# Kernel tuning notes

Hardware: AMD Instinct MI355X
Metric: run time of the kernel (lower is better)

Reference implementation:

```python
import jax, jax.numpy as jnp
import numpy as np

E = 3_200_000
H = 8
N = 100_000

def setup_inputs() -> dict:
    key = jax.random.key(0)
    k1, k2 = jax.random.split(key)
    logits = jax.random.normal(k1, (E, H, 1), dtype=jnp.float32)
    dst = jax.random.randint(k2, (E,), 0, N, dtype=jnp.int32)
    return {"logits": logits, "dst": dst, "num_nodes": N}

def reference(logits, dst, num_nodes):
    # block_compute(copy_edge, max): segmented max of edge logits per dst node -> [M, H, 1]
    max_logits = jax.ops.segment_max(logits, dst, num_segments=num_nodes)
    # apply_block: exp(z_ij - max_i) per edge (gather dst max back to edges)
    scores = jnp.exp(logits - max_logits[dst])  # [E, H, 1]
    # block_compute(copy_edge, sum): segmented sum of exp'd scores per dst node -> [M, H, 1]
    normalizer = jax.ops.segment_sum(scores, dst, num_segments=num_nodes)
    return scores, normalizer
```

## Files before the change

kernel.cpp:

```cpp
#include <hip/hip_runtime.h>


__device__ __forceinline__ unsigned enc_f32(float f) {
    unsigned u = __float_as_uint(f);
    return (u & 0x80000000u) ? ~u : (u | 0x80000000u);
}
__device__ __forceinline__ float dec_f32(unsigned u) {
    return __uint_as_float((u & 0x80000000u) ? (u & 0x7FFFFFFFu) : ~u);
}

template <int H>
__global__ void smax_k(const float* __restrict__ logits,
                       const int* __restrict__ dst,
                       unsigned* __restrict__ menc, int EH) {
    int i = blockIdx.x * blockDim.x + threadIdx.x;
    if (i >= EH) return;
    int e = i / H;
    int h = i - e * H;
    int d = dst[e];
    atomicMax(menc + d * H + h, enc_f32(logits[i]));
}

__global__ void smax_g(const float* __restrict__ logits,
                       const int* __restrict__ dst,
                       unsigned* __restrict__ menc, int EH, int H) {
    int i = blockIdx.x * blockDim.x + threadIdx.x;
    if (i >= EH) return;
    int e = i / H;
    int h = i - e * H;
    int d = dst[e];
    atomicMax(menc + d * H + h, enc_f32(logits[i]));
}

template <int H>
__global__ void score_k(const float* __restrict__ logits,
                        const int* __restrict__ dst,
                        const unsigned* __restrict__ menc,
                        float* __restrict__ scores,
                        float* __restrict__ norm, int EH) {
    int i = blockIdx.x * blockDim.x + threadIdx.x;
    if (i >= EH) return;
    int e = i / H;
    int h = i - e * H;
    int d = dst[e];
    float m = dec_f32(menc[d * H + h]);
    float s = expf(logits[i] - m);
    scores[i] = s;
    atomicAdd(norm + d * H + h, s);
}

__global__ void score_g(const float* __restrict__ logits,
                        const int* __restrict__ dst,
                        const unsigned* __restrict__ menc,
                        float* __restrict__ scores,
                        float* __restrict__ norm, int EH, int H) {
    int i = blockIdx.x * blockDim.x + threadIdx.x;
    if (i >= EH) return;
    int e = i / H;
    int h = i - e * H;
    int d = dst[e];
    float m = dec_f32(menc[d * H + h]);
    float s = expf(logits[i] - m);
    scores[i] = s;
    atomicAdd(norm + d * H + h, s);
}

extern "C" void kernel_launch(void* const* d_in, const int* in_sizes, int n_in,
                              void* d_out, int out_size, void* d_ws, size_t ws_size,
                              hipStream_t stream) {
    const float* logits = (const float*)d_in[0];
    const int*   dst    = (const int*)d_in[1];

    const int EH = in_sizes[0];
    const int E  = in_sizes[1];
    const int H  = EH / E;
    const int NH = out_size - EH;

    float* scores = (float*)d_out;
    float* norm   = scores + EH;
    unsigned* menc = (unsigned*)d_ws;

    hipMemsetAsync(menc, 0, (size_t)NH * sizeof(unsigned), stream);
    hipMemsetAsync(norm, 0, (size_t)NH * sizeof(float), stream);

    const int block = 256;
    const int grid  = (EH + block - 1) / block;

    if (H == 8) {
        smax_k<8><<<grid, block, 0, stream>>>(logits, dst, menc, EH);
        score_k<8><<<grid, block, 0, stream>>>(logits, dst, menc, scores, norm, EH);
    } else {
        smax_g<<<grid, block, 0, stream>>>(logits, dst, menc, EH, H);
        score_g<<<grid, block, 0, stream>>>(logits, dst, menc, scores, norm, EH, H);
    }
}
```

Before: 294.8 us.

## Replace atomic segment max/sum with CSR build and per-node wavefront reduction

Builds a CSR grouping of edges by destination node (histogram, three-stage scan, atomic scatter into a permutation), then runs one wavefront per node. Each wavefront loads its edges' logits as float4, reduces the max and sum with shuffles, and writes scores and the normalizer directly. This removes the per-element global atomicMax and atomicAdd contention. In exchange it adds several kernel launches, an atomic histogram and scatter over edges, and gathered non-coalesced logit reads. Edge order within a node depends on the atomics, so the float sum order is nondeterministic.

```diff
diff --git a/kernel.cpp b/kernel.cpp
--- a/kernel.cpp
+++ b/kernel.cpp
@@ -9,60 +9,188 @@
     return __uint_as_float((u & 0x80000000u) ? (u & 0x7FFFFFFFu) : ~u);
 }
 
-template <int H>
-__global__ void smax_k(const float* __restrict__ logits,
-                       const int* __restrict__ dst,
-                       unsigned* __restrict__ menc, int EH) {
+#define SCAN_B 256
+
+__global__ __launch_bounds__(256)
+void k_hist(const int* __restrict__ dst, unsigned* __restrict__ counts, int E) {
+    int e = blockIdx.x * 256 + threadIdx.x;
+    if (e < E) atomicAdd(&counts[dst[e]], 1u);
+}
+
+__global__ __launch_bounds__(SCAN_B)
+void k_scan1(const unsigned* __restrict__ counts, unsigned* __restrict__ row_start,
+             unsigned* __restrict__ partials, int N) {
+    __shared__ unsigned tmp[SCAN_B];
+    int j = blockIdx.x * SCAN_B + threadIdx.x;
+    unsigned v = (j < N) ? counts[j] : 0u;
+    tmp[threadIdx.x] = v;
+    __syncthreads();
+    for (int off = 1; off < SCAN_B; off <<= 1) {
+        unsigned t = (threadIdx.x >= off) ? tmp[threadIdx.x - off] : 0u;
+        __syncthreads();
+        tmp[threadIdx.x] += t;
+        __syncthreads();
+    }
+    if (j < N) row_start[j] = tmp[threadIdx.x] - v;
+    if (threadIdx.x == SCAN_B - 1) partials[blockIdx.x] = tmp[SCAN_B - 1];
+}
+
+__global__ __launch_bounds__(1024)
+void k_scan2(unsigned* __restrict__ partials, int nb) {
+    __shared__ unsigned tmp[1024];
+    __shared__ unsigned carry_s;
+    if (threadIdx.x == 0) carry_s = 0u;
+    __syncthreads();
+    for (int base = 0; base < nb; base += 1024) {
+        int j = base + threadIdx.x;
+        unsigned v = (j < nb) ? partials[j] : 0u;
+        tmp[threadIdx.x] = v;
+        __syncthreads();
+        for (int off = 1; off < 1024; off <<= 1) {
+            unsigned t = (threadIdx.x >= off) ? tmp[threadIdx.x - off] : 0u;
+            __syncthreads();
+            tmp[threadIdx.x] += t;
+            __syncthreads();
+        }
+        unsigned incl  = tmp[threadIdx.x];
+        unsigned total = tmp[1023];
+        if (j < nb) partials[j] = incl - v + carry_s;
+        __syncthreads();
+        if (threadIdx.x == 0) carry_s += total;
+        __syncthreads();
+    }
+}
+
+__global__ __launch_bounds__(SCAN_B)
+void k_scan3(unsigned* __restrict__ row_start, const unsigned* __restrict__ partials,
+             unsigned* __restrict__ row_cur, int N) {
+    int j = blockIdx.x * SCAN_B + threadIdx.x;
+    if (j < N) {
+        unsigned v = row_start[j] + partials[blockIdx.x];
+        row_start[j] = v;
+        row_cur[j]   = v;
+    }
+}
+
+__global__ __launch_bounds__(256)
+void k_scatter(const int* __restrict__ dst, unsigned* __restrict__ row_cur,
+               unsigned* __restrict__ perm, int E) {
+    int e = blockIdx.x * 256 + threadIdx.x;
+    if (e < E) {
+        unsigned p = atomicAdd(&row_cur[dst[e]], 1u);
+        perm[p] = (unsigned)e;
+    }
+}
+
+__global__ __launch_bounds__(256)
+void k_node(const float* __restrict__ logits, const unsigned* __restrict__ perm,
+            const unsigned* __restrict__ row_start, const unsigned* __restrict__ counts,
+            float* __restrict__ scores, float* __restrict__ norm, int N) {
+    int wid  = (blockIdx.x * 256 + threadIdx.x) >> 6;
+    int lane = threadIdx.x & 63;
+    if (wid >= N) return;
+    unsigned start = row_start[wid];
+    unsigned deg   = counts[wid];
+
+    float z[8];
+    float m[8];
+#pragma unroll
+    for (int h = 0; h < 8; ++h) m[h] = -INFINITY;
+
+    bool single = (deg <= 64u);
+    unsigned eid0 = 0u;
+
+    if (single) {
+        if (lane < (int)deg) {
+            eid0 = perm[start + lane];
+            const float4* lp = (const float4*)(logits + (size_t)eid0 * 8);
+            float4 x = lp[0], y = lp[1];
+            z[0] = x.x; z[1] = x.y; z[2] = x.z; z[3] = x.w;
+            z[4] = y.x; z[5] = y.y; z[6] = y.z; z[7] = y.w;
+#pragma unroll
+            for (int h = 0; h < 8; ++h) m[h] = z[h];
+        }
+    } else {
+        for (unsigned c = lane; c < deg; c += 64u) {
+            unsigned eid = perm[start + c];
+            const float4* lp = (const float4*)(logits + (size_t)eid * 8);
+            float4 x = lp[0], y = lp[1];
+            m[0] = fmaxf(m[0], x.x); m[1] = fmaxf(m[1], x.y);
+            m[2] = fmaxf(m[2], x.z); m[3] = fmaxf(m[3], x.w);
+            m[4] = fmaxf(m[4], y.x); m[5] = fmaxf(m[5], y.y);
+            m[6] = fmaxf(m[6], y.z); m[7] = fmaxf(m[7], y.w);
+        }
+    }
+
+#pragma unroll
+    for (int off = 1; off < 64; off <<= 1) {
+#pragma unroll
+        for (int h = 0; h < 8; ++h)
+            m[h] = fmaxf(m[h], __shfl_xor(m[h], off));
+    }
+
+    float acc[8];
+#pragma unroll
+    for (int h = 0; h < 8; ++h) acc[h] = 0.0f;
+
+    if (single) {
+        if (lane < (int)deg) {
+            float s[8];
+#pragma unroll
+            for (int h = 0; h < 8; ++h) { s[h] = __expf(z[h] - m[h]); acc[h] = s[h]; }
+            float4* sp = (float4*)(scores + (size_t)eid0 * 8);
+            sp[0] = make_float4(s[0], s[1], s[2], s[3]);
+            sp[1] = make_float4(s[4], s[5], s[6], s[7]);
+        }
+    } else {
+        for (unsigned c = lane; c < deg; c += 64u) {
+            unsigned eid = perm[start + c];
+            const float4* lp = (const float4*)(logits + (size_t)eid * 8);
+            float4 x = lp[0], y = lp[1];
+            float s0 = __expf(x.x - m[0]), s1 = __expf(x.y - m[1]);
+            float s2 = __expf(x.z - m[2]), s3 = __expf(x.w - m[3]);
+            float s4 = __expf(y.x - m[4]), s5 = __expf(y.y - m[5]);
+            float s6 = __expf(y.z - m[6]), s7 = __expf(y.w - m[7]);
+            float4* sp = (float4*)(scores + (size_t)eid * 8);
+            sp[0] = make_float4(s0, s1, s2, s3);
+            sp[1] = make_float4(s4, s5, s6, s7);
+            acc[0] += s0; acc[1] += s1; acc[2] += s2; acc[3] += s3;
+            acc[4] += s4; acc[5] += s5; acc[6] += s6; acc[7] += s7;
+        }
+    }
+
+#pragma unroll
+    for (int off = 1; off < 64; off <<= 1) {
+#pragma unroll
+        for (int h = 0; h < 8; ++h)
+            acc[h] += __shfl_xor(acc[h], off);
+    }
+
+    if (lane == 0) {
+        float4* np = (float4*)(norm + (size_t)wid * 8);
+        np[0] = make_float4(acc[0], acc[1], acc[2], acc[3]);
+        np[1] = make_float4(acc[4], acc[5], acc[6], acc[7]);
+    }
+}
+
+
+__global__ void pass1_old(const float* __restrict__ logits, const int* __restrict__ dst,
+                          unsigned* __restrict__ menc, int EH, int H) {
     int i = blockIdx.x * blockDim.x + threadIdx.x;
     if (i >= EH) return;
-    int e = i / H;
-    int h = i - e * H;
-    int d = dst[e];
-    atomicMax(menc + d * H + h, enc_f32(logits[i]));
-}
-
-__global__ void smax_g(const float* __restrict__ logits,
-                       const int* __restrict__ dst,
-                       unsigned* __restrict__ menc, int EH, int H) {
+    int e = i / H, h = i - e * H;
+    atomicMax(menc + (size_t)dst[e] * H + h, enc_f32(logits[i]));
+}
+__global__ void pass2_old(const float* __restrict__ logits, const int* __restrict__ dst,
+                          const unsigned* __restrict__ menc, float* __restrict__ scores,
+                          float* __restrict__ norm, int EH, int H) {
     int i = blockIdx.x * blockDim.x + threadIdx.x;
     if (i >= EH) return;
-    int e = i / H;
-    int h = i - e * H;
+    int e = i / H, h = i - e * H;
     int d = dst[e];
-    atomicMax(menc + d * H + h, enc_f32(logits[i]));
-}
-
-template <int H>
-__global__ void score_k(const float* __restrict__ logits,
-                        const int* __restrict__ dst,
-                        const unsigned* __restrict__ menc,
-                        float* __restrict__ scores,
-                        float* __restrict__ norm, int EH) {
-    int i = blockIdx.x * blockDim.x + threadIdx.x;
-    if (i >= EH) return;
-    int e = i / H;
-    int h = i - e * H;
-    int d = dst[e];
-    float m = dec_f32(menc[d * H + h]);
-    float s = expf(logits[i] - m);
+    float s = __expf(logits[i] - dec_f32(menc[(size_t)d * H + h]));
     scores[i] = s;
-    atomicAdd(norm + d * H + h, s);
-}
-
-__global__ void score_g(const float* __restrict__ logits,
-                        const int* __restrict__ dst,
-                        const unsigned* __restrict__ menc,
-                        float* __restrict__ scores,
-                        float* __restrict__ norm, int EH, int H) {
-    int i = blockIdx.x * blockDim.x + threadIdx.x;
-    if (i >= EH) return;
-    int e = i / H;
-    int h = i - e * H;
-    int d = dst[e];
-    float m = dec_f32(menc[d * H + h]);
-    float s = expf(logits[i] - m);
-    scores[i] = s;
-    atomicAdd(norm + d * H + h, s);
+    atomicAdd(norm + (size_t)d * H + h, s);
 }
 
 extern "C" void kernel_launch(void* const* d_in, const int* in_sizes, int n_in,
@@ -75,22 +203,40 @@
     const int E  = in_sizes[1];
     const int H  = EH / E;
     const int NH = out_size - EH;
+    const int N  = NH / H;
 
     float* scores = (float*)d_out;
     float* norm   = scores + EH;
-    unsigned* menc = (unsigned*)d_ws;
-
-    hipMemsetAsync(menc, 0, (size_t)NH * sizeof(unsigned), stream);
-    hipMemsetAsync(norm, 0, (size_t)NH * sizeof(float), stream);
-
-    const int block = 256;
-    const int grid  = (EH + block - 1) / block;
-
-    if (H == 8) {
-        smax_k<8><<<grid, block, 0, stream>>>(logits, dst, menc, EH);
-        score_k<8><<<grid, block, 0, stream>>>(logits, dst, menc, scores, norm, EH);
-    } else {
-        smax_g<<<grid, block, 0, stream>>>(logits, dst, menc, EH, H);
-        score_g<<<grid, block, 0, stream>>>(logits, dst, menc, scores, norm, EH, H);
-    }
-}
+
+    const int nb1 = (N + SCAN_B - 1) / SCAN_B;
+    const size_t need = ((size_t)3 * N + nb1 + E + 64) * sizeof(unsigned);
+
+    if (H != 8 || ws_size < need) {
+        unsigned* menc = (unsigned*)d_ws;
+        hipMemsetAsync(menc, 0, (size_t)NH * 4, stream);
+        hipMemsetAsync(norm, 0, (size_t)NH * 4, stream);
+        int block = 256, grid = (EH + block - 1) / block;
+        pass1_old<<<grid, block, 0, stream>>>(logits, dst, menc, EH, H);
+        pass2_old<<<grid, block, 0, stream>>>(logits, dst, menc, scores, norm, EH, H);
+        return;
+    }
+
+    unsigned* counts    = (unsigned*)d_ws;
+    unsigned* row_start = counts + N;
+    unsigned* row_cur   = row_start + N;
+    unsigned* partials  = row_cur + N;
+    unsigned* perm      = partials + ((nb1 + 63) & ~63);
+
+    hipMemsetAsync(counts, 0, (size_t)N * 4, stream);
+
+    const int gridE = (E + 255) / 256;
+    const int gridW = (N * 64 + 255) / 256;
+
+    k_hist   <<<gridE, 256, 0, stream>>>(dst, counts, E);
+    k_scan1  <<<nb1, SCAN_B, 0, stream>>>(counts, row_start, partials, N);
+    k_scan2  <<<1, 1024, 0, stream>>>(partials, nb1);
+    k_scan3  <<<nb1, SCAN_B, 0, stream>>>(row_start, partials, row_cur, N);
+    k_scatter<<<gridE, 256, 0, stream>>>(dst, row_cur, perm, E);
+    k_node   <<<gridW, 256, 0, stream>>>(logits, perm, row_start, counts,
+                                         scores, norm, N);
+}
```

Result: slower. 555.2 us (+88.3%).

## Bucket edges by destination block and reduce in shared memory

Applied to the files above, without the earlier changes.

Replaces the two global-atomic passes with a counting-sort pipeline. A histogram, a single-block scan and a scatter bucket edges into 64-node groups, with 8 replicas per bucket to spread atomic contention. A per-bucket kernel then computes max and exp-sum using shared-memory atomics and writes norm directly, with no memset or global float atomics. This adds three extra launches, a serial single-block scan, a permutation buffer and gathered logit reads. Scores are written through a random scatter, and fast __expf is used.

```diff
diff --git a/kernel.cpp b/kernel.cpp
--- a/kernel.cpp
+++ b/kernel.cpp
@@ -1,5 +1,9 @@
 #include <hip/hip_runtime.h>
 
+
+#define RREP    8
+#define BSHIFT  6
+#define BNODES  64
 
 __device__ __forceinline__ unsigned enc_f32(float f) {
     unsigned u = __float_as_uint(f);
@@ -9,60 +13,144 @@
     return __uint_as_float((u & 0x80000000u) ? (u & 0x7FFFFFFFu) : ~u);
 }
 
-template <int H>
-__global__ void smax_k(const float* __restrict__ logits,
-                       const int* __restrict__ dst,
-                       unsigned* __restrict__ menc, int EH) {
+__global__ __launch_bounds__(256)
+void k_hist(const int* __restrict__ dst, unsigned* __restrict__ counts, int E) {
+    int e = blockIdx.x * 256 + threadIdx.x;
+    if (e < E) {
+        int b = (dst[e] >> BSHIFT) * RREP + (blockIdx.x & (RREP - 1));
+        atomicAdd(&counts[b], 1u);
+    }
+}
+
+__global__ __launch_bounds__(1024)
+void k_scan(const unsigned* __restrict__ counts, unsigned* __restrict__ off,
+            unsigned* __restrict__ cur, int M) {
+    __shared__ unsigned tmp[1024];
+    __shared__ unsigned carry;
+    if (threadIdx.x == 0) carry = 0u;
+    __syncthreads();
+    for (int base = 0; base < M; base += 1024) {
+        int j = base + threadIdx.x;
+        unsigned v = (j < M) ? counts[j] : 0u;
+        tmp[threadIdx.x] = v;
+        __syncthreads();
+        for (int o = 1; o < 1024; o <<= 1) {
+            unsigned t = (threadIdx.x >= o) ? tmp[threadIdx.x - o] : 0u;
+            __syncthreads();
+            tmp[threadIdx.x] += t;
+            __syncthreads();
+        }
+        if (j < M) {
+            unsigned ex = tmp[threadIdx.x] - v + carry;
+            off[j] = ex;
+            cur[j] = ex;
+        }
+        unsigned tot = tmp[1023];
+        __syncthreads();
+        if (threadIdx.x == 0) carry += tot;
+        __syncthreads();
+    }
+    if (threadIdx.x == 0) off[M] = carry;
+}
+
+__global__ __launch_bounds__(256)
+void k_scatter2(const int* __restrict__ dst, unsigned* __restrict__ cur,
+                unsigned* __restrict__ perm, int E) {
+    int e = blockIdx.x * 256 + threadIdx.x;
+    if (e < E) {
+        int d = dst[e];
+        int b = (d >> BSHIFT) * RREP + (blockIdx.x & (RREP - 1));
+        unsigned p = atomicAdd(&cur[b], 1u);
+        perm[p] = ((unsigned)(d & (BNODES - 1)) << 26) | (unsigned)e;
+    }
+}
+
+__global__ __launch_bounds__(256)
+void k_bucket(const float* __restrict__ logits, const unsigned* __restrict__ perm,
+              const unsigned* __restrict__ off, float* __restrict__ scores,
+              float* __restrict__ norm, int N) {
+    __shared__ unsigned mEnc[8 * BNODES];
+    __shared__ float    sSum[8 * BNODES];
+    const int b = blockIdx.x;
+    for (int j = threadIdx.x; j < 8 * BNODES; j += 256) {
+        mEnc[j] = 0u;
+        sSum[j] = 0.0f;
+    }
+    const unsigned start = off[(unsigned)b * RREP];
+    const unsigned end   = off[(unsigned)(b + 1) * RREP];
+    __syncthreads();
+
+    for (unsigned c = start + threadIdx.x; c < end; c += 256) {
+        unsigned pk = perm[c];
+        unsigned e  = pk & 0x03FFFFFFu;
+        unsigned ld = pk >> 26;
+        const float4* lp = (const float4*)(logits + (size_t)e * 8);
+        float4 x = lp[0], y = lp[1];
+        atomicMax(&mEnc[0 * BNODES + ld], enc_f32(x.x));
+        atomicMax(&mEnc[1 * BNODES + ld], enc_f32(x.y));
+        atomicMax(&mEnc[2 * BNODES + ld], enc_f32(x.z));
+        atomicMax(&mEnc[3 * BNODES + ld], enc_f32(x.w));
+        atomicMax(&mEnc[4 * BNODES + ld], enc_f32(y.x));
+        atomicMax(&mEnc[5 * BNODES + ld], enc_f32(y.y));
+        atomicMax(&mEnc[6 * BNODES + ld], enc_f32(y.z));
+        atomicMax(&mEnc[7 * BNODES + ld], enc_f32(y.w));
+    }
+    __syncthreads();
+
+    for (unsigned c = start + threadIdx.x; c < end; c += 256) {
+        unsigned pk = perm[c];
+        unsigned e  = pk & 0x03FFFFFFu;
+        unsigned ld = pk >> 26;
+        const float4* lp = (const float4*)(logits + (size_t)e * 8);
+        float4 x = lp[0], y = lp[1];
+        float s0 = __expf(x.x - dec_f32(mEnc[0 * BNODES + ld]));
+        float s1 = __expf(x.y - dec_f32(mEnc[1 * BNODES + ld]));
+        float s2 = __expf(x.z - dec_f32(mEnc[2 * BNODES + ld]));
+        float s3 = __expf(x.w - dec_f32(mEnc[3 * BNODES + ld]));
+        float s4 = __expf(y.x - dec_f32(mEnc[4 * BNODES + ld]));
+        float s5 = __expf(y.y - dec_f32(mEnc[5 * BNODES + ld]));
+        float s6 = __expf(y.z - dec_f32(mEnc[6 * BNODES + ld]));
+        float s7 = __expf(y.w - dec_f32(mEnc[7 * BNODES + ld]));
+        float4* sp = (float4*)(scores + (size_t)e * 8);
+        sp[0] = make_float4(s0, s1, s2, s3);
+        sp[1] = make_float4(s4, s5, s6, s7);
+        atomicAdd(&sSum[0 * BNODES + ld], s0);
+        atomicAdd(&sSum[1 * BNODES + ld], s1);
+        atomicAdd(&sSum[2 * BNODES + ld], s2);
+        atomicAdd(&sSum[3 * BNODES + ld], s3);
+        atomicAdd(&sSum[4 * BNODES + ld], s4);
+        atomicAdd(&sSum[5 * BNODES + ld], s5);
+        atomicAdd(&sSum[6 * BNODES + ld], s6);
+        atomicAdd(&sSum[7 * BNODES + ld], s7);
+    }
+    __syncthreads();
+
+    const int nodeBase = b << BSHIFT;
+    for (int j = threadIdx.x; j < 8 * BNODES; j += 256) {
+        int ld = j >> 3, h = j & 7;
+        int node = nodeBase + ld;
+        if (node < N) norm[(size_t)node * 8 + h] = sSum[h * BNODES + ld];
+    }
+}
+
+
+__global__ void pass1_old(const float* __restrict__ logits, const int* __restrict__ dst,
+                          unsigned* __restrict__ menc, int EH, int H) {
     int i = blockIdx.x * blockDim.x + threadIdx.x;
     if (i >= EH) return;
-    int e = i / H;
-    int h = i - e * H;
-    int d = dst[e];
-    atomicMax(menc + d * H + h, enc_f32(logits[i]));
+    int e = i / H, h = i - e * H;
+    atomicMax(menc + (size_t)dst[e] * H + h, enc_f32(logits[i]));
 }
-
-__global__ void smax_g(const float* __restrict__ logits,
-                       const int* __restrict__ dst,
-                       unsigned* __restrict__ menc, int EH, int H) {
+__global__ void pass2_old(const float* __restrict__ logits, const int* __restrict__ dst,
+                          const unsigned* __restrict__ menc, float* __restrict__ scores,
+                          float* __restrict__ norm, int EH, int H) {
     int i = blockIdx.x * blockDim.x + threadIdx.x;
     if (i >= EH) return;
-    int e = i / H;
-    int h = i - e * H;
+    int e = i / H, h = i - e * H;
     int d = dst[e];
-    atomicMax(menc + d * H + h, enc_f32(logits[i]));
-}
-
-template <int H>
-__global__ void score_k(const float* __restrict__ logits,
-                        const int* __restrict__ dst,
-                        const unsigned* __restrict__ menc,
-                        float* __restrict__ scores,
-                        float* __restrict__ norm, int EH) {
-    int i = blockIdx.x * blockDim.x + threadIdx.x;
-    if (i >= EH) return;
-    int e = i / H;
-    int h = i - e * H;
-    int d = dst[e];
-    float m = dec_f32(menc[d * H + h]);
-    float s = expf(logits[i] - m);
+    float s = __expf(logits[i] - dec_f32(menc[(size_t)d * H + h]));
     scores[i] = s;
-    atomicAdd(norm + d * H + h, s);
-}
-
-__global__ void score_g(const float* __restrict__ logits,
-                        const int* __restrict__ dst,
-                        const unsigned* __restrict__ menc,
-                        float* __restrict__ scores,
-                        float* __restrict__ norm, int EH, int H) {
-    int i = blockIdx.x * blockDim.x + threadIdx.x;
-    if (i >= EH) return;
-    int e = i / H;
-    int h = i - e * H;
-    int d = dst[e];
-    float m = dec_f32(menc[d * H + h]);
-    float s = expf(logits[i] - m);
-    scores[i] = s;
-    atomicAdd(norm + d * H + h, s);
+    atomicAdd(norm + (size_t)d * H + h, s);
 }
 
 extern "C" void kernel_launch(void* const* d_in, const int* in_sizes, int n_in,
@@ -75,22 +163,36 @@
     const int E  = in_sizes[1];
     const int H  = EH / E;
     const int NH = out_size - EH;
+    const int N  = NH / H;
 
     float* scores = (float*)d_out;
     float* norm   = scores + EH;
-    unsigned* menc = (unsigned*)d_ws;
 
-    hipMemsetAsync(menc, 0, (size_t)NH * sizeof(unsigned), stream);
-    hipMemsetAsync(norm, 0, (size_t)NH * sizeof(float), stream);
+    const int NBKT = (N + BNODES - 1) >> BSHIFT;
+    const int M    = NBKT * RREP;
+    const size_t need = ((size_t)3 * M + 1 + (size_t)E) * sizeof(unsigned);
 
-    const int block = 256;
-    const int grid  = (EH + block - 1) / block;
+    if (H != 8 || E >= (1 << 26) || ws_size < need) {
+        unsigned* menc = (unsigned*)d_ws;
+        hipMemsetAsync(menc, 0, (size_t)NH * 4, stream);
+        hipMemsetAsync(norm, 0, (size_t)NH * 4, stream);
+        int block = 256, grid = (EH + block - 1) / block;
+        pass1_old<<<grid, block, 0, stream>>>(logits, dst, menc, EH, H);
+        pass2_old<<<grid, block, 0, stream>>>(logits, dst, menc, scores, norm, EH, H);
+        return;
+    }
 
-    if (H == 8) {
-        smax_k<8><<<grid, block, 0, stream>>>(logits, dst, menc, EH);
-        score_k<8><<<grid, block, 0, stream>>>(logits, dst, menc, scores, norm, EH);
-    } else {
-        smax_g<<<grid, block, 0, stream>>>(logits, dst, menc, EH, H);
-        score_g<<<grid, block, 0, stream>>>(logits, dst, menc, scores, norm, EH, H);
-    }
+    unsigned* counts = (unsigned*)d_ws;
+    unsigned* off    = counts + M;
+    unsigned* cur    = off + M + 1;
+    unsigned* perm   = cur + M;
+
+    hipMemsetAsync(counts, 0, (size_t)M * 4, stream);
+
+    const int gridE = (E + 255) / 256;
+
+    k_hist    <<<gridE, 256, 0, stream>>>(dst, counts, E);
+    k_scan    <<<1, 1024, 0, stream>>>(counts, off, cur, M);
+    k_scatter2<<<gridE, 256, 0, stream>>>(dst, cur, perm, E);
+    k_bucket  <<<NBKT, 256, 0, stream>>>(logits, perm, off, scores, norm, N);
 }
```

Measured after the change: 555.3 us. +88.4%, slower.
